# Kernel tuning notes

Hardware: AMD Instinct MI355X
Metric: run time of the kernel (lower is better)

The kernel has to match this reference:

```python
import jax, jax.numpy as jnp
import numpy as np
import math

TOP_K = 10  # top-k codes kept by SOHO_Pre_VD for negative sampling
EPS_LN = 1e-5


def layer_norm(x, w, b):
    mu = jnp.mean(x, axis=-1, keepdims=True)
    var = jnp.mean((x - mu) ** 2, axis=-1, keepdims=True)
    return (x - mu) * jax.lax.rsqrt(var + EPS_LN) * w + b


def position_encoding_sine(b, l, d):
    # mask is all-ones [b, l]; identical across batch, compute once and broadcast
    h = w = int(math.sqrt(l))
    ones = jnp.ones((h, w), jnp.float32)
    y_embed = jnp.cumsum(ones, axis=0)
    x_embed = jnp.cumsum(ones, axis=1)
    eps = 1e-6
    two_pi = 2.0 * np.pi
    y_embed = y_embed / (y_embed[-1:, :] + eps) * two_pi
    x_embed = x_embed / (x_embed[:, -1:] + eps) * two_pi
    pf = d // 2
    dim_t = jnp.arange(pf, dtype=jnp.float32)
    dim_t = 10000.0 ** (2.0 * jnp.floor(dim_t / 2.0) / pf)
    px = x_embed[:, :, None] / dim_t  # [h, w, pf]
    py = y_embed[:, :, None] / dim_t
    # interleave sin(even), cos(odd)
    px = jnp.stack([jnp.sin(px[..., 0::2]), jnp.cos(px[..., 1::2])], axis=-1).reshape(h, w, pf)
    py = jnp.stack([jnp.sin(py[..., 0::2]), jnp.cos(py[..., 1::2])], axis=-1).reshape(h, w, pf)
    pos = jnp.concatenate([py, px], axis=-1).reshape(l, d)  # [l, d]
    return jnp.broadcast_to(pos, (b, l, d))


def setup_inputs() -> dict:
    key = jax.random.key(0)
    ks = jax.random.split(key, 10)
    B, L, CIN, D, K = 16, 576, 1024, 768, 8192
    s = 0.02
    return {
        "img": jax.random.normal(ks[0], (B, L, CIN), jnp.float32),
        "mask_indices": jax.random.randint(ks[1], (B, 1), 0, L),
        "lin_w": jax.random.normal(ks[2], (D, CIN), jnp.float32) * s,
        "lin_b": jnp.zeros((D,), jnp.float32),
        "ln1_w": jnp.ones((D,), jnp.float32),
        "ln1_b": jnp.zeros((D,), jnp.float32),
        "embed": jax.random.normal(ks[3], (K, D), jnp.float32),
        "pos_w": jax.random.normal(ks[4], (D, D), jnp.float32) * s,
        "pos_b": jnp.zeros((D,), jnp.float32),
        "gate_w": jax.random.normal(ks[5], (2, 2 * D), jnp.float32) * s,
        "gate_b": jnp.zeros((2,), jnp.float32),
        "gate_ln_w": jnp.ones((2,), jnp.float32),
        "gate_ln_b": jnp.zeros((2,), jnp.float32),
        "out_ln_w": jnp.ones((D,), jnp.float32),
        "out_ln_b": jnp.zeros((D,), jnp.float32),
    }


def reference(img, mask_indices, lin_w, lin_b, ln1_w, ln1_b, embed, pos_w, pos_b,
              gate_w, gate_b, gate_ln_w, gate_ln_b, out_ln_w, out_ln_b):
    b, l, _ = img.shape
    d = lin_w.shape[0]
    # self.linear: Linear -> LayerNorm -> ReLU
    xq = jax.nn.relu(layer_norm(img @ lin_w.T + lin_b, ln1_w, ln1_b))  # [b,l,d]
    x = xq.reshape(b * l, d)
    # SOHO VQ: nearest code by L2, straight-through
    d2 = (x * x).sum(-1, keepdims=True) - 2.0 * (x @ embed.T) + (embed * embed).sum(-1)  # [N,K]
    idx = jnp.argmin(d2, axis=-1)  # [N]
    quant = jnp.take(embed, idx, axis=0)
    quantized = x + jax.lax.stop_gradient(quant - x)
    probs = jax.nn.softmax(-d2, axis=-1)
    topk_values, topk_indices = jax.lax.top_k(probs, TOP_K)  # [N,K'],[N,K']
    # pos_align linear
    quantized = quantized @ pos_w.T + pos_b
    emb_pt = quantized.reshape(b, l, d)
    # gated fusion
    g = jnp.concatenate([emb_pt, xq], axis=-1) @ gate_w.T + gate_b  # [b,l,2]
    g = jax.nn.relu(layer_norm(g, gate_ln_w, gate_ln_b))
    score = jax.nn.softmax(g, axis=-1)
    emb_s, img_s = score[..., 0:1], score[..., 1:2]
    emb_pt = emb_pt * emb_s + xq * img_s
    pos = position_encoding_sine(b, l, d)
    # negative index construction (visual_mask is all ones)
    ind = idx.reshape(b, l).astype(jnp.float32)  # [b,l]
    masked_labels = jnp.take_along_axis(ind, mask_indices, axis=1)  # [b,1]
    masked_neg = (ind == masked_labels).astype(jnp.float32)[..., None]  # [b,l,1]
    samp = jax.random.categorical(jax.random.key(42), jnp.log(topk_values))  # [N]
    neg = jnp.take_along_axis(topk_indices, samp[:, None], axis=1).reshape(b, l, 1).astype(jnp.float32)
    neg_at_mask = jnp.take_along_axis(neg[..., 0], mask_indices, axis=1)[..., None]  # [b,1,1]
    neg_idx = neg_at_mask * masked_neg + ind[..., None] * (1.0 - masked_neg)  # [b,l,1]
    neg_idx = neg_idx.reshape(b * l).astype(jnp.int32)
    # one-hot matmul == embedding gather
    neg_q = jnp.take(embed, neg_idx, axis=0).reshape(b, l, d)
    neg_q = neg_q * emb_s + jax.lax.stop_gradient(xq) * img_s
    out_pos = layer_norm(emb_pt + pos, out_ln_w, out_ln_b)
    out_neg = layer_norm(neg_q + pos, out_ln_w, out_ln_b)
    return (out_pos, out_neg)
```

## Files before the change

### kernel.cpp

```cpp
#include <hip/hip_runtime.h>
#include <stdint.h>

#define M_TOT  9216
#define D_     768
#define CIN_   1024
#define KCODE  8192
#define TOPK   10

typedef unsigned short u16;
typedef __bf16 bf16x8 __attribute__((ext_vector_type(8)));
typedef float f32x4 __attribute__((ext_vector_type(4)));


__device__ inline float block_sum(float v, float* red) {
    int t = threadIdx.x;
    red[t] = v;
    __syncthreads();
    #pragma unroll
    for (int s = 128; s > 0; s >>= 1) {
        if (t < s) red[t] += red[t + s];
        __syncthreads();
    }
    float r = red[0];
    __syncthreads();
    return r;
}

__device__ inline unsigned long long umin64(unsigned long long a, unsigned long long b) {
    return (a < b) ? a : b;
}

__device__ inline u16 f2bf(float f) {
    uint32_t u = __float_as_uint(f);
    uint32_t r = (u + 0x7fffu + ((u >> 16) & 1u)) >> 16;
    return (u16)r;
}
__device__ inline float bf2f(u16 h) {
    return __uint_as_float(((uint32_t)h) << 16);
}

__device__ inline unsigned long long shfl_xor_u64(unsigned long long v, int mask) {
    int lo = (int)(uint32_t)v, hi = (int)(uint32_t)(v >> 32);
    lo = __shfl_xor(lo, mask, 64);
    hi = __shfl_xor(hi, mask, 64);
    return ((unsigned long long)(uint32_t)hi << 32) | (uint32_t)lo;
}

#define GLDS(gp, lp) __builtin_amdgcn_global_load_lds( \
    (const __attribute__((address_space(1))) unsigned int*)(gp), \
    (__attribute__((address_space(3))) unsigned int*)(lp), 16, 0, 0)


__global__ __launch_bounds__(256) void k_gemm1_mfma(
    const u16* __restrict__ Ah, const u16* __restrict__ Am, const u16* __restrict__ Al,
    const u16* __restrict__ Bh, const u16* __restrict__ Bm, const u16* __restrict__ Bl,
    const float* __restrict__ bias, float* __restrict__ C)
{
    __shared__ __align__(16) u16 sm[24576];
    const int t = threadIdx.x;
    const int lane = t & 63, wid = t >> 6;
    const int row0 = blockIdx.y * 128, col0 = blockIdx.x * 128;
    const int r16 = lane & 15, kb = lane >> 4;
    const int wr = wid >> 1, wc = wid & 1;
    const int sc = (((lane & 3) ^ ((lane >> 3) & 3))) * 8;
    const int lrow = lane >> 2;
    const int swz = (r16 >> 1) & 3;

    f32x4 acc[4][4];
    #pragma unroll
    for (int mf = 0; mf < 4; ++mf)
        #pragma unroll
        for (int nf = 0; nf < 4; ++nf)
            acc[mf][nf] = (f32x4){0.f, 0.f, 0.f, 0.f};

    for (int k0 = 0; k0 < CIN_; k0 += 32) {
        __syncthreads();
        #pragma unroll
        for (int i = 0; i < 12; ++i) {
            int mat = i >> 1;
            int c = (i & 1) ? wid + 4 : wid;
            const u16* mp = (mat == 0) ? Ah : (mat == 1) ? Am : (mat == 2) ? Al
                          : (mat == 3) ? Bh : (mat == 4) ? Bm : Bl;
            int rbase = (mat < 3) ? row0 : col0;
            const u16* g = mp + (size_t)(rbase + c * 16 + lrow) * CIN_ + k0 + sc;
            GLDS(g, sm + mat * 4096 + c * 512);
        }
        __syncthreads();

        const int slot = (kb ^ swz) * 8;
        bf16x8 bh[4], bm[4], bl[4];
        #pragma unroll
        for (int nf = 0; nf < 4; ++nf) {
            int offb = 12288 + (wc * 64 + nf * 16 + r16) * 32 + slot;
            bh[nf] = *(const bf16x8*)(sm + offb);
            bm[nf] = *(const bf16x8*)(sm + offb + 4096);
            bl[nf] = *(const bf16x8*)(sm + offb + 8192);
        }
        #pragma unroll
        for (int mf = 0; mf < 4; ++mf) {
            int offa = (wr * 64 + mf * 16 + r16) * 32 + slot;
            bf16x8 ah = *(const bf16x8*)(sm + offa);
            bf16x8 am = *(const bf16x8*)(sm + offa + 4096);
            bf16x8 al = *(const bf16x8*)(sm + offa + 8192);
            #pragma unroll
            for (int nf = 0; nf < 4; ++nf) {
                acc[mf][nf] = __builtin_amdgcn_mfma_f32_16x16x32_bf16(ah, bh[nf], acc[mf][nf], 0, 0, 0);
                acc[mf][nf] = __builtin_amdgcn_mfma_f32_16x16x32_bf16(ah, bm[nf], acc[mf][nf], 0, 0, 0);
                acc[mf][nf] = __builtin_amdgcn_mfma_f32_16x16x32_bf16(am, bh[nf], acc[mf][nf], 0, 0, 0);
                acc[mf][nf] = __builtin_amdgcn_mfma_f32_16x16x32_bf16(am, bm[nf], acc[mf][nf], 0, 0, 0);
                acc[mf][nf] = __builtin_amdgcn_mfma_f32_16x16x32_bf16(ah, bl[nf], acc[mf][nf], 0, 0, 0);
                acc[mf][nf] = __builtin_amdgcn_mfma_f32_16x16x32_bf16(al, bh[nf], acc[mf][nf], 0, 0, 0);
            }
        }
    }

    #pragma unroll
    for (int mf = 0; mf < 4; ++mf) {
        #pragma unroll
        for (int q = 0; q < 4; ++q) {
            int m = row0 + wr * 64 + mf * 16 + kb * 4 + q;
            #pragma unroll
            for (int nf = 0; nf < 4; ++nf) {
                int n = col0 + wc * 64 + nf * 16 + r16;
                C[(size_t)m * D_ + n] = acc[mf][nf][q] + bias[n];
            }
        }
    }
}

__global__ __launch_bounds__(256) void k_gemm3_mfma(
    const u16* __restrict__ Eh, const u16* __restrict__ El,
    const u16* __restrict__ Ph, const u16* __restrict__ Pl,
    const int* __restrict__ gather,
    const float* __restrict__ bias, float* __restrict__ C)
{
    __shared__ __align__(16) u16 sm[2][16384];
    const int t = threadIdx.x;
    const int lane = t & 63, wid = t >> 6;
    const int row0 = blockIdx.y * 128, col0 = blockIdx.x * 128;
    const int r16 = lane & 15, kb = lane >> 4;
    const int wr = wid >> 1, wc = wid & 1;
    const int sc = (((lane & 3) ^ ((lane >> 3) & 3))) * 8;
    const int lrow = lane >> 2;
    const int swz = (r16 >> 1) & 3;

    const u16* sb = (wid == 0) ? Eh : (wid == 1) ? El : (wid == 2) ? Ph : Pl;
    int grow[8];
    #pragma unroll
    for (int c = 0; c < 8; ++c) {
        int r = ((wid < 2) ? row0 : col0) + c * 16 + lrow;
        grow[c] = (wid < 2) ? gather[r] : r;
    }

    f32x4 acc[4][4];
    #pragma unroll
    for (int mf = 0; mf < 4; ++mf)
        #pragma unroll
        for (int nf = 0; nf < 4; ++nf)
            acc[mf][nf] = (f32x4){0.f, 0.f, 0.f, 0.f};

    auto STAGE = [&](int buf, int k0) {
        u16* dst = sm[buf] + wid * 4096 + lane * 8;
        #pragma unroll
        for (int c = 0; c < 8; ++c)
            GLDS(sb + (size_t)grow[c] * D_ + k0 + sc, dst + c * 512);
    };

    STAGE(0, 0);
    __syncthreads();
    for (int kt = 0; kt < 24; ++kt) {
        int cur = kt & 1;
        if (kt < 23) STAGE(cur ^ 1, (kt + 1) * 32);
        const u16* B = sm[cur];
        const int slot = (kb ^ swz) * 8;
        bf16x8 bh[4], bl[4];
        #pragma unroll
        for (int nf = 0; nf < 4; ++nf) {
            int off = 8192 + (wc * 64 + nf * 16 + r16) * 32 + slot;
            bh[nf] = *(const bf16x8*)(B + off);
            bl[nf] = *(const bf16x8*)(B + off + 4096);
        }
        #pragma unroll
        for (int mf = 0; mf < 4; ++mf) {
            int off = (wr * 64 + mf * 16 + r16) * 32 + slot;
            bf16x8 ah = *(const bf16x8*)(B + off);
            bf16x8 al = *(const bf16x8*)(B + off + 4096);
            #pragma unroll
            for (int nf = 0; nf < 4; ++nf) {
                acc[mf][nf] = __builtin_amdgcn_mfma_f32_16x16x32_bf16(ah, bh[nf], acc[mf][nf], 0, 0, 0);
                acc[mf][nf] = __builtin_amdgcn_mfma_f32_16x16x32_bf16(ah, bl[nf], acc[mf][nf], 0, 0, 0);
                acc[mf][nf] = __builtin_amdgcn_mfma_f32_16x16x32_bf16(al, bh[nf], acc[mf][nf], 0, 0, 0);
            }
        }
        __syncthreads();
    }

    #pragma unroll
    for (int mf = 0; mf < 4; ++mf) {
        #pragma unroll
        for (int q = 0; q < 4; ++q) {
            int m = row0 + wr * 64 + mf * 16 + kb * 4 + q;
            #pragma unroll
            for (int nf = 0; nf < 4; ++nf) {
                int n = col0 + wc * 64 + nf * 16 + r16;
                C[(size_t)m * D_ + n] = acc[mf][nf][q] + bias[n];
            }
        }
    }
}

__global__ void k_rowflag(const int* __restrict__ mask, int* __restrict__ rowflag)
{
    int i = blockIdx.x * 256 + threadIdx.x;
    if (i < M_TOT) {
        int b = i / 576, l = i - b * 576;
        rowflag[i] = (mask[b] == l) ? (b + 1) : 0;
    }
}

__global__ __launch_bounds__(256) void k_gemm2_mfma(
    const u16* __restrict__ Xh, const u16* __restrict__ Xl,
    const u16* __restrict__ Eh, const u16* __restrict__ El,
    const float* __restrict__ xsq, const float* __restrict__ esq,
    const int* __restrict__ rowflag, float* __restrict__ d2row,
    unsigned long long* __restrict__ amin)
{
    __shared__ __align__(16) u16 sm[2][16384];
    const int t = threadIdx.x;
    const int lane = t & 63, wid = t >> 6;
    const int row0 = blockIdx.y * 128, col0 = blockIdx.x * 128;
    const int r16 = lane & 15, kb = lane >> 4;
    const int wr = wid >> 1, wc = wid & 1;
    const int sc = (((lane & 3) ^ ((lane >> 3) & 3))) * 8;
    const int lrow = lane >> 2;
    const int swz = (r16 >> 1) & 3;

    f32x4 acc[4][4];
    #pragma unroll
    for (int mf = 0; mf < 4; ++mf)
        #pragma unroll
        for (int nf = 0; nf < 4; ++nf)
            acc[mf][nf] = (f32x4){0.f, 0.f, 0.f, 0.f};

    const u16* sb = (wid == 0) ? Xh : (wid == 1) ? Xl : (wid == 2) ? Eh : El;
    const int rbase = (wid < 2) ? row0 : col0;
    const u16* srcb = sb + (size_t)(rbase + lrow) * D_ + sc;

    auto STAGE = [&](int buf, int k0) {
        u16* dst = sm[buf] + wid * 4096 + lane * 8;
        #pragma unroll
        for (int c = 0; c < 8; ++c)
            GLDS(srcb + (size_t)c * 16 * D_ + k0, dst + c * 512);
    };

    STAGE(0, 0);
    __syncthreads();
    for (int kt = 0; kt < 24; ++kt) {
        int cur = kt & 1;
        if (kt < 23) STAGE(cur ^ 1, (kt + 1) * 32);
        const u16* B = sm[cur];
        const int slot = (kb ^ swz) * 8;
        bf16x8 bh[4], bl[4];
        #pragma unroll
        for (int nf = 0; nf < 4; ++nf) {
            int off = 8192 + (wc * 64 + nf * 16 + r16) * 32 + slot;
            bh[nf] = *(const bf16x8*)(B + off);
            bl[nf] = *(const bf16x8*)(B + off + 4096);
        }
        #pragma unroll
        for (int mf = 0; mf < 4; ++mf) {
            int off = (wr * 64 + mf * 16 + r16) * 32 + slot;
            bf16x8 ah = *(const bf16x8*)(B + off);
            bf16x8 al = *(const bf16x8*)(B + off + 4096);
            #pragma unroll
            for (int nf = 0; nf < 4; ++nf) {
                acc[mf][nf] = __builtin_amdgcn_mfma_f32_16x16x32_bf16(ah, bh[nf], acc[mf][nf], 0, 0, 0);
                acc[mf][nf] = __builtin_amdgcn_mfma_f32_16x16x32_bf16(ah, bl[nf], acc[mf][nf], 0, 0, 0);
                acc[mf][nf] = __builtin_amdgcn_mfma_f32_16x16x32_bf16(al, bh[nf], acc[mf][nf], 0, 0, 0);
            }
        }
        __syncthreads();
    }

    float esqv[4];
    #pragma unroll
    for (int nf = 0; nf < 4; ++nf)
        esqv[nf] = esq[col0 + wc * 64 + nf * 16 + r16];

    #pragma unroll
    for (int mf = 0; mf < 4; ++mf) {
        #pragma unroll
        for (int q = 0; q < 4; ++q) {
            int m = row0 + wr * 64 + mf * 16 + kb * 4 + q;
            float xsv = xsq[m];
            int rf = rowflag[m];
            unsigned long long best = ~0ull;
            #pragma unroll
            for (int nf = 0; nf < 4; ++nf) {
                int n = col0 + wc * 64 + nf * 16 + r16;
                float d2 = (xsv - 2.0f * acc[mf][nf][q]) + esqv[nf];
                if (rf) d2row[(size_t)(rf - 1) * KCODE + n] = d2;
                unsigned long long key =
                    ((unsigned long long)__float_as_uint(d2) << 32) | (unsigned)n;
                best = umin64(best, key);
            }
            #pragma unroll
            for (int msk = 1; msk < 16; msk <<= 1)
                best = umin64(best, shfl_xor_u64(best, msk));
            if (r16 == 0) atomicMin(&amin[m], best);
        }
    }
}

__global__ __launch_bounds__(256) void k_split3(const float* __restrict__ in,
    u16* __restrict__ h, u16* __restrict__ m, u16* __restrict__ l, int n4)
{
    int i = blockIdx.x * 256 + threadIdx.x;
    int stride = gridDim.x * 256;
    for (; i < n4; i += stride) {
        float4 v = ((const float4*)in)[i];
        ushort4 hv, mv, lv;
        float x, r;
        x = v.x; hv.x = f2bf(x); r = x - bf2f(hv.x); mv.x = f2bf(r); lv.x = f2bf(r - bf2f(mv.x));
        x = v.y; hv.y = f2bf(x); r = x - bf2f(hv.y); mv.y = f2bf(r); lv.y = f2bf(r - bf2f(mv.y));
        x = v.z; hv.z = f2bf(x); r = x - bf2f(hv.z); mv.z = f2bf(r); lv.z = f2bf(r - bf2f(mv.z));
        x = v.w; hv.w = f2bf(x); r = x - bf2f(hv.w); mv.w = f2bf(r); lv.w = f2bf(r - bf2f(mv.w));
        ((ushort4*)h)[i] = hv; ((ushort4*)m)[i] = mv; ((ushort4*)l)[i] = lv;
    }
}

__global__ __launch_bounds__(256) void k_split2(const float* __restrict__ in,
    u16* __restrict__ h, u16* __restrict__ l, int n4)
{
    int i = blockIdx.x * 256 + threadIdx.x;
    int stride = gridDim.x * 256;
    for (; i < n4; i += stride) {
        float4 v = ((const float4*)in)[i];
        ushort4 hv, lv;
        hv.x = f2bf(v.x); lv.x = f2bf(v.x - bf2f(hv.x));
        hv.y = f2bf(v.y); lv.y = f2bf(v.y - bf2f(hv.y));
        hv.z = f2bf(v.z); lv.z = f2bf(v.z - bf2f(hv.z));
        hv.w = f2bf(v.w); lv.w = f2bf(v.w - bf2f(hv.w));
        ((ushort4*)h)[i] = hv; ((ushort4*)l)[i] = lv;
    }
}

__global__ __launch_bounds__(256) void k_ln_relu(
    const float* __restrict__ in, const float* __restrict__ w,
    const float* __restrict__ b, float* __restrict__ xq, float* __restrict__ xsq,
    u16* __restrict__ Xh, u16* __restrict__ Xl)
{
    __shared__ float red[256];
    int r = blockIdx.x, t = threadIdx.x;
    const float* row = in + (size_t)r * D_;
    float v0 = row[t], v1 = row[t + 256], v2 = row[t + 512];
    float mu = block_sum(v0 + v1 + v2, red) * (1.0f / 768.0f);
    float d0 = v0 - mu, d1 = v1 - mu, d2 = v2 - mu;
    float var = block_sum(d0 * d0 + d1 * d1 + d2 * d2, red) * (1.0f / 768.0f);
    float rn = 1.0f / sqrtf(var + 1e-5f);
    float o0 = fmaxf(0.0f, d0 * rn * w[t] + b[t]);
    float o1 = fmaxf(0.0f, d1 * rn * w[t + 256] + b[t + 256]);
    float o2 = fmaxf(0.0f, d2 * rn * w[t + 512] + b[t + 512]);
    float* orow = xq + (size_t)r * D_;
    orow[t] = o0; orow[t + 256] = o1; orow[t + 512] = o2;
    u16 h0 = f2bf(o0), h1 = f2bf(o1), h2 = f2bf(o2);
    Xh[(size_t)r * D_ + t]       = h0;
    Xh[(size_t)r * D_ + t + 256] = h1;
    Xh[(size_t)r * D_ + t + 512] = h2;
    Xl[(size_t)r * D_ + t]       = f2bf(o0 - bf2f(h0));
    Xl[(size_t)r * D_ + t + 256] = f2bf(o1 - bf2f(h1));
    Xl[(size_t)r * D_ + t + 512] = f2bf(o2 - bf2f(h2));
    float q = block_sum(o0 * o0 + o1 * o1 + o2 * o2, red);
    if (t == 0) xsq[r] = q;
}

__global__ __launch_bounds__(256) void k_esq(const float* __restrict__ E,
                                             float* __restrict__ esq,
                                             u16* __restrict__ Eh,
                                             u16* __restrict__ El)
{
    __shared__ float red[256];
    int r = blockIdx.x, t = threadIdx.x;
    const float* row = E + (size_t)r * D_;
    float v0 = row[t], v1 = row[t + 256], v2 = row[t + 512];
    u16 h0 = f2bf(v0), h1 = f2bf(v1), h2 = f2bf(v2);
    Eh[(size_t)r * D_ + t]       = h0;
    Eh[(size_t)r * D_ + t + 256] = h1;
    Eh[(size_t)r * D_ + t + 512] = h2;
    El[(size_t)r * D_ + t]       = f2bf(v0 - bf2f(h0));
    El[(size_t)r * D_ + t + 256] = f2bf(v1 - bf2f(h1));
    El[(size_t)r * D_ + t + 512] = f2bf(v2 - bf2f(h2));
    float s = block_sum(v0 * v0 + v1 * v1 + v2 * v2, red);
    if (t == 0) esq[r] = s;
}

__global__ void k_extract(const unsigned long long* __restrict__ amin,
                          int* __restrict__ idx, int n)
{
    int i = blockIdx.x * 256 + threadIdx.x;
    if (i < n) idx[i] = (int)(amin[i] & 0xFFFFFFFFull);
}

__global__ __launch_bounds__(256) void k_gate(
    const float* __restrict__ embpt, const float* __restrict__ xq,
    const float* __restrict__ gw, const float* __restrict__ gb,
    const float* __restrict__ glnw, const float* __restrict__ glnb,
    float* __restrict__ scores)
{
    __shared__ float red[256];
    int r = blockIdx.x, t = threadIdx.x;
    const float* ep = embpt + (size_t)r * D_;
    const float* xr = xq + (size_t)r * D_;
    float g0 = 0.0f, g1 = 0.0f;
    for (int k = t; k < 1536; k += 256) {
        float v = (k < 768) ? ep[k] : xr[k - 768];
        g0 = fmaf(v, gw[k], g0);
        g1 = fmaf(v, gw[1536 + k], g1);
    }
    g0 = block_sum(g0, red);
    g1 = block_sum(g1, red);
    if (t == 0) {
        g0 += gb[0]; g1 += gb[1];
        float mu = 0.5f * (g0 + g1);
        float h0 = g0 - mu, h1 = g1 - mu;
        float var = 0.5f * (h0 * h0 + h1 * h1);
        float rn = 1.0f / sqrtf(var + 1e-5f);
        float o0 = fmaxf(0.0f, h0 * rn * glnw[0] + glnb[0]);
        float o1 = fmaxf(0.0f, h1 * rn * glnw[1] + glnb[1]);
        float m = fmaxf(o0, o1);
        float e0 = expf(o0 - m), e1 = expf(o1 - m);
        float inv = 1.0f / (e0 + e1);
        scores[r * 2 + 0] = e0 * inv;
        scores[r * 2 + 1] = e1 * inv;
    }
}

__global__ __launch_bounds__(256) void k_pos(float* __restrict__ pos)
{
    int l = blockIdx.x, t = threadIdx.x;
    for (int k = t; k < D_; k += 256) {
        int kk = (k < 384) ? k : k - 384;
        int m = kk >> 1;
        float coord = (k < 384) ? (float)(l / 24) : (float)(l % 24);
        float v = (coord + 1.0f) / 24.000001f * 6.28318530717958647692f;
        float tm = exp2f((float)m * (13.287712379549449f / 192.0f));
        float a = v / tm;
        pos[(size_t)l * D_ + k] = (kk & 1) ? cosf(a) : sinf(a);
    }
}

__device__ inline void threefry2x32(uint32_t x0, uint32_t x1,
                                    uint32_t& o0, uint32_t& o1)
{
    const uint32_t ks0 = 0u, ks1 = 42u;
    const uint32_t ks2 = ks0 ^ ks1 ^ 0x1BD11BDAu;
    uint32_t ks[3] = {ks0, ks1, ks2};
    x0 += ks[0]; x1 += ks[1];
    const int R0[4] = {13, 15, 26, 6};
    const int R1[4] = {17, 29, 16, 24};
    #pragma unroll
    for (int i = 0; i < 5; ++i) {
        const int* R = (i & 1) ? R1 : R0;
        #pragma unroll
        for (int q = 0; q < 4; ++q) {
            x0 += x1;
            x1 = (x1 << R[q]) | (x1 >> (32 - R[q]));
            x1 ^= x0;
        }
        x0 += ks[(i + 1) % 3];
        x1 += ks[(i + 2) % 3] + (uint32_t)(i + 1);
    }
    o0 = x0; o1 = x1;
}

__global__ __launch_bounds__(256) void k_topk_sample(
    const float* __restrict__ d2row, const unsigned long long* __restrict__ amin,
    const int* __restrict__ mask, int* __restrict__ mlabel, int* __restrict__ negsel)
{
    __shared__ float sd2[KCODE];
    __shared__ unsigned long long rbuf[256];
    __shared__ float rfs[256];
    __shared__ int sel[TOPK];
    __shared__ float selv[TOPK];
    __shared__ float sS;
    int b = blockIdx.x, t = threadIdx.x;
    for (int j = t; j < KCODE; j += 256) sd2[j] = d2row[b * KCODE + j];
    __syncthreads();
    for (int p = 0; p < TOPK; ++p) {
        unsigned long long best = ~0ull;
        for (int j = t; j < KCODE; j += 256) {
            bool skip = false;
            for (int q = 0; q < p; ++q) skip = skip || (j == sel[q]);
            if (skip) continue;
            unsigned long long key =
                ((unsigned long long)__float_as_uint(sd2[j]) << 32) | (unsigned)j;
            best = umin64(best, key);
        }
        rbuf[t] = best;
        __syncthreads();
        for (int s = 128; s > 0; s >>= 1) {
            if (t < s) rbuf[t] = umin64(rbuf[t], rbuf[t + s]);
            __syncthreads();
        }
        if (t == 0) {
            sel[p] = (int)(rbuf[0] & 0xFFFFFFFFull);
            selv[p] = __uint_as_float((uint32_t)(rbuf[0] >> 32));
        }
        __syncthreads();
    }
    float d2min = selv[0];
    float part = 0.0f;
    for (int j = t; j < KCODE; j += 256) part += expf(d2min - sd2[j]);
    part = block_sum(part, rfs);
    if (t == 0) sS = part;
    __syncthreads();
    if (t == 0) {
        int rb = b * 576 + mask[b];
        mlabel[b] = (int)(amin[rb] & 0xFFFFFFFFull);
        float S = sS;
        float bestv = 0.0f;
        int samp = 0;
        bool first = true;
        for (int k = 0; k < TOPK; ++k) {
            float pk = expf(d2min - selv[k]) / S;
            float logit = logf(pk);
            unsigned f = (unsigned)(rb * 10 + k);
            uint32_t o0, o1;
            threefry2x32(0u, f, o0, o1);
            uint32_t bits = o0 ^ o1;
            float uu = __uint_as_float(0x3F800000u | (bits >> 9)) - 1.0f;
            uu = uu + 1.1754944e-38f;
            uu = fmaxf(1.1754944e-38f, uu);
            float gum = -logf(-logf(uu));
            float sc = logit + gum;
            if (first || sc > bestv) { bestv = sc; samp = k; first = false; }
        }
        negsel[b] = sel[samp];
    }
}

__global__ __launch_bounds__(256) void k_final(
    const float* __restrict__ embpt, const float* __restrict__ xq,
    const float* __restrict__ scores, const int* __restrict__ idx,
    const int* __restrict__ mlabel, const int* __restrict__ negsel,
    const float* __restrict__ E, const float* __restrict__ pos,
    const float* __restrict__ ow, const float* __restrict__ ob,
    float* __restrict__ outp, float* __restrict__ outn)
{
    __shared__ float red[256];
    int r = blockIdx.x, t = threadIdx.x;
    int b = r / 576, l = r % 576;
    float s0 = scores[r * 2 + 0], s1 = scores[r * 2 + 1];
    int ir = idx[r];
    int nidx = (ir == mlabel[b]) ? negsel[b] : ir;
    const float* ep = embpt + (size_t)r * D_;
    const float* xr = xq + (size_t)r * D_;
    const float* er = E + (size_t)nidx * D_;
    const float* pr = pos + (size_t)l * D_;
    float vp[3], vn[3];
    #pragma unroll
    for (int q = 0; q < 3; ++q) {
        int k = t + q * 256;
        float xv = xr[k] * s1;
        float pv = pr[k];
        vp[q] = (ep[k] * s0 + xv) + pv;
        vn[q] = (er[k] * s0 + xv) + pv;
    }
    float mup = block_sum(vp[0] + vp[1] + vp[2], red) * (1.0f / 768.0f);
    float a0 = vp[0] - mup, a1 = vp[1] - mup, a2 = vp[2] - mup;
    float varp = block_sum(a0 * a0 + a1 * a1 + a2 * a2, red) * (1.0f / 768.0f);
    float rnp = 1.0f / sqrtf(varp + 1e-5f);
    float mun = block_sum(vn[0] + vn[1] + vn[2], red) * (1.0f / 768.0f);
    float c0 = vn[0] - mun, c1 = vn[1] - mun, c2 = vn[2] - mun;
    float varn = block_sum(c0 * c0 + c1 * c1 + c2 * c2, red) * (1.0f / 768.0f);
    float rnn = 1.0f / sqrtf(varn + 1e-5f);
    float* op = outp + (size_t)r * D_;
    float* on = outn + (size_t)r * D_;
    op[t]       = a0 * rnp * ow[t]       + ob[t];
    op[t + 256] = a1 * rnp * ow[t + 256] + ob[t + 256];
    op[t + 512] = a2 * rnp * ow[t + 512] + ob[t + 512];
    on[t]       = c0 * rnn * ow[t]       + ob[t];
    on[t + 256] = c1 * rnn * ow[t + 256] + ob[t + 256];
    on[t + 512] = c2 * rnn * ow[t + 512] + ob[t + 512];
}

extern "C" void kernel_launch(void* const* d_in, const int* in_sizes, int n_in,
                              void* d_out, int out_size, void* d_ws, size_t ws_size,
                              hipStream_t stream)
{
    (void)in_sizes; (void)n_in; (void)out_size; (void)ws_size;
    const float* img    = (const float*)d_in[0];
    const int*   maski  = (const int*)d_in[1];
    const float* lin_w  = (const float*)d_in[2];
    const float* lin_b  = (const float*)d_in[3];
    const float* ln1_w  = (const float*)d_in[4];
    const float* ln1_b  = (const float*)d_in[5];
    const float* embed  = (const float*)d_in[6];
    const float* pos_w  = (const float*)d_in[7];
    const float* pos_b  = (const float*)d_in[8];
    const float* gate_w = (const float*)d_in[9];
    const float* gate_b = (const float*)d_in[10];
    const float* glnw   = (const float*)d_in[11];
    const float* glnb   = (const float*)d_in[12];
    const float* olnw   = (const float*)d_in[13];
    const float* olnb   = (const float*)d_in[14];

    uint8_t* wp = (uint8_t*)d_ws;
    auto alloc = [&](size_t bytes) -> void* {
        void* p = (void*)wp;
        wp += (bytes + 255) & ~(size_t)255;
        return p;
    };
    float* bufA = (float*)alloc((size_t)M_TOT * D_ * 4);
    float* xq   = (float*)alloc((size_t)M_TOT * D_ * 4);
    float* xsq  = (float*)alloc((size_t)M_TOT * 4);
    float* esq  = (float*)alloc((size_t)KCODE * 4);
    unsigned long long* amin = (unsigned long long*)alloc((size_t)M_TOT * 8);
    int*   idxA   = (int*)alloc((size_t)M_TOT * 4);
    int*   rowflag = (int*)alloc((size_t)M_TOT * 4);
    float* scores = (float*)alloc((size_t)M_TOT * 2 * 4);
    float* posb   = (float*)alloc((size_t)576 * D_ * 4);
    float* d2row  = (float*)alloc((size_t)16 * KCODE * 4);
    int*   mlab   = (int*)alloc(16 * 4);
    int*   negsel = (int*)alloc(16 * 4);
    u16* Wh = (u16*)alloc((size_t)D_ * CIN_ * 2);
    u16* Wm = (u16*)alloc((size_t)D_ * CIN_ * 2);
    u16* Wl = (u16*)alloc((size_t)D_ * CIN_ * 2);
    u16* Ph = (u16*)alloc((size_t)D_ * D_ * 2);
    u16* Pl = (u16*)alloc((size_t)D_ * D_ * 2);
    u16* R  = (u16*)alloc((size_t)3 * M_TOT * CIN_ * 2);
    u16* Ih = R;
    u16* Im = R + (size_t)M_TOT * CIN_;
    u16* Il = R + (size_t)2 * M_TOT * CIN_;
    u16* Xh = R;
    u16* Xl = Xh + (size_t)M_TOT * D_;
    u16* Eh = Xl + (size_t)M_TOT * D_;
    u16* El = Eh + (size_t)KCODE * D_;

    float* outp = (float*)d_out;
    float* outn = outp + (size_t)M_TOT * D_;

    hipMemsetAsync(amin, 0xFF, M_TOT * sizeof(unsigned long long), stream);

    dim3 blk(256);
    k_split3<<<2048, blk, 0, stream>>>(img, Ih, Im, Il, M_TOT * CIN_ / 4);
    k_split3<<<768, blk, 0, stream>>>(lin_w, Wh, Wm, Wl, D_ * CIN_ / 4);
    k_split2<<<576, blk, 0, stream>>>(pos_w, Ph, Pl, D_ * D_ / 4);
    k_rowflag<<<M_TOT / 256, blk, 0, stream>>>(maski, rowflag);
    k_gemm1_mfma<<<dim3(D_ / 128, M_TOT / 128), blk, 0, stream>>>(
        Ih, Im, Il, Wh, Wm, Wl, lin_b, bufA);
    k_ln_relu<<<M_TOT, blk, 0, stream>>>(bufA, ln1_w, ln1_b, xq, xsq, Xh, Xl);
    k_esq<<<KCODE, blk, 0, stream>>>(embed, esq, Eh, El);
    k_gemm2_mfma<<<dim3(KCODE / 128, M_TOT / 128), blk, 0, stream>>>(
        Xh, Xl, Eh, El, xsq, esq, rowflag, d2row, amin);
    k_extract<<<M_TOT / 256, blk, 0, stream>>>(amin, idxA, M_TOT);
    k_gemm3_mfma<<<dim3(D_ / 128, M_TOT / 128), blk, 0, stream>>>(
        Eh, El, Ph, Pl, idxA, pos_b, bufA);
    k_gate<<<M_TOT, blk, 0, stream>>>(bufA, xq, gate_w, gate_b, glnw, glnb, scores);
    k_pos<<<576, blk, 0, stream>>>(posb);
    k_topk_sample<<<16, blk, 0, stream>>>(d2row, amin, maski, mlab, negsel);
    k_final<<<M_TOT, blk, 0, stream>>>(bufA, xq, scores, idxA, mlab, negsel,
                                       embed, posb, olnw, olnb, outp, outn);
}
```

Measured before the change: 791.1 us.

## Widen gemm2 K-tile to 64 single-buffered and fuse small prep kernels

The distance GEMM now stages 64-wide K slices into one 64KB LDS buffer, using an 8-way XOR swizzle and two sync points per iteration. This replaces the 32-wide double-buffered pipeline and halves the number of loop iterations and barriers, but loads no longer overlap with compute. Separately, the weight splits and the rowflag kernel are merged into one k_prep launch to cut launch overhead.

```diff
diff --git a/kernel.cpp b/kernel.cpp
--- a/kernel.cpp
+++ b/kernel.cpp
@@ -49,7 +49,6 @@
 #define GLDS(gp, lp) __builtin_amdgcn_global_load_lds( \
     (const __attribute__((address_space(1))) unsigned int*)(gp), \
     (__attribute__((address_space(3))) unsigned int*)(lp), 16, 0, 0)
-
 
 __global__ __launch_bounds__(256) void k_gemm1_mfma(
     const u16* __restrict__ Ah, const u16* __restrict__ Am, const u16* __restrict__ Al,
@@ -209,15 +208,6 @@
     }
 }
 
-__global__ void k_rowflag(const int* __restrict__ mask, int* __restrict__ rowflag)
-{
-    int i = blockIdx.x * 256 + threadIdx.x;
-    if (i < M_TOT) {
-        int b = i / 576, l = i - b * 576;
-        rowflag[i] = (mask[b] == l) ? (b + 1) : 0;
-    }
-}
-
 __global__ __launch_bounds__(256) void k_gemm2_mfma(
     const u16* __restrict__ Xh, const u16* __restrict__ Xl,
     const u16* __restrict__ Eh, const u16* __restrict__ El,
@@ -225,15 +215,12 @@
     const int* __restrict__ rowflag, float* __restrict__ d2row,
     unsigned long long* __restrict__ amin)
 {
-    __shared__ __align__(16) u16 sm[2][16384];
+    __shared__ __align__(16) u16 sm[32768];
     const int t = threadIdx.x;
     const int lane = t & 63, wid = t >> 6;
     const int row0 = blockIdx.y * 128, col0 = blockIdx.x * 128;
     const int r16 = lane & 15, kb = lane >> 4;
     const int wr = wid >> 1, wc = wid & 1;
-    const int sc = (((lane & 3) ^ ((lane >> 3) & 3))) * 8;
-    const int lrow = lane >> 2;
-    const int swz = (r16 >> 1) & 3;
 
     f32x4 acc[4][4];
     #pragma unroll
@@ -244,42 +231,41 @@
 
     const u16* sb = (wid == 0) ? Xh : (wid == 1) ? Xl : (wid == 2) ? Eh : El;
     const int rbase = (wid < 2) ? row0 : col0;
-    const u16* srcb = sb + (size_t)(rbase + lrow) * D_ + sc;
-
-    auto STAGE = [&](int buf, int k0) {
-        u16* dst = sm[buf] + wid * 4096 + lane * 8;
-        #pragma unroll
-        for (int c = 0; c < 8; ++c)
-            GLDS(srcb + (size_t)c * 16 * D_ + k0, dst + c * 512);
-    };
-
-    STAGE(0, 0);
-    __syncthreads();
-    for (int kt = 0; kt < 24; ++kt) {
-        int cur = kt & 1;
-        if (kt < 23) STAGE(cur ^ 1, (kt + 1) * 32);
-        const u16* B = sm[cur];
-        const int slot = (kb ^ swz) * 8;
-        bf16x8 bh[4], bl[4];
-        #pragma unroll
-        for (int nf = 0; nf < 4; ++nf) {
-            int off = 8192 + (wc * 64 + nf * 16 + r16) * 32 + slot;
-            bh[nf] = *(const bf16x8*)(B + off);
-            bl[nf] = *(const bf16x8*)(B + off + 4096);
-        }
-        #pragma unroll
-        for (int mf = 0; mf < 4; ++mf) {
-            int off = (wr * 64 + mf * 16 + r16) * 32 + slot;
-            bf16x8 ah = *(const bf16x8*)(B + off);
-            bf16x8 al = *(const bf16x8*)(B + off + 4096);
+    const u16* srcb = sb + (size_t)(rbase + (lane >> 3)) * D_
+                         + ((lane & 7) ^ (lane >> 3)) * 8;
+    u16* dstb = sm + wid * 8192 + lane * 8;
+
+    const int swz = (r16 & 7);
+    for (int kt = 0; kt < 12; ++kt) {
+        __syncthreads();
+        #pragma unroll
+        for (int c = 0; c < 16; ++c) {
+            GLDS(srcb + kt * 64 + c * 8 * D_, dstb + c * 512);
+        }
+        __syncthreads();
+        #pragma unroll
+        for (int h = 0; h < 2; ++h) {
+            const int slot = ((h * 4 + kb) ^ swz) * 8;
+            bf16x8 bh[4], bl[4];
             #pragma unroll
             for (int nf = 0; nf < 4; ++nf) {
-                acc[mf][nf] = __builtin_amdgcn_mfma_f32_16x16x32_bf16(ah, bh[nf], acc[mf][nf], 0, 0, 0);
-                acc[mf][nf] = __builtin_amdgcn_mfma_f32_16x16x32_bf16(ah, bl[nf], acc[mf][nf], 0, 0, 0);
-                acc[mf][nf] = __builtin_amdgcn_mfma_f32_16x16x32_bf16(al, bh[nf], acc[mf][nf], 0, 0, 0);
+                int off = (wc * 64 + nf * 16 + r16) * 64 + slot;
+                bh[nf] = *(const bf16x8*)(sm + 16384 + off);
+                bl[nf] = *(const bf16x8*)(sm + 24576 + off);
             }
-        }
-        __syncthreads();
+            #pragma unroll
+            for (int mf = 0; mf < 4; ++mf) {
+                int off = (wr * 64 + mf * 16 + r16) * 64 + slot;
+                bf16x8 ah = *(const bf16x8*)(sm + off);
+                bf16x8 al = *(const bf16x8*)(sm + 8192 + off);
+                #pragma unroll
+                for (int nf = 0; nf < 4; ++nf) {
+                    acc[mf][nf] = __builtin_amdgcn_mfma_f32_16x16x32_bf16(ah, bh[nf], acc[mf][nf], 0, 0, 0);
+                    acc[mf][nf] = __builtin_amdgcn_mfma_f32_16x16x32_bf16(ah, bl[nf], acc[mf][nf], 0, 0, 0);
+                    acc[mf][nf] = __builtin_amdgcn_mfma_f32_16x16x32_bf16(al, bh[nf], acc[mf][nf], 0, 0, 0);
+                }
+            }
+        }
     }
 
     float esqv[4];
@@ -329,19 +315,36 @@
     }
 }
 
-__global__ __launch_bounds__(256) void k_split2(const float* __restrict__ in,
-    u16* __restrict__ h, u16* __restrict__ l, int n4)
-{
-    int i = blockIdx.x * 256 + threadIdx.x;
-    int stride = gridDim.x * 256;
-    for (; i < n4; i += stride) {
-        float4 v = ((const float4*)in)[i];
+__global__ __launch_bounds__(256) void k_prep(
+    const float* __restrict__ lin_w, u16* __restrict__ Wh, u16* __restrict__ Wm,
+    u16* __restrict__ Wl,
+    const float* __restrict__ pos_w, u16* __restrict__ Ph, u16* __restrict__ Pl,
+    const int* __restrict__ mask, int* __restrict__ rowflag)
+{
+    int bid = blockIdx.x;
+    if (bid < 768) {
+        int i = bid * 256 + threadIdx.x;
+        float4 v = ((const float4*)lin_w)[i];
+        ushort4 hv, mv, lv;
+        float x, r;
+        x = v.x; hv.x = f2bf(x); r = x - bf2f(hv.x); mv.x = f2bf(r); lv.x = f2bf(r - bf2f(mv.x));
+        x = v.y; hv.y = f2bf(x); r = x - bf2f(hv.y); mv.y = f2bf(r); lv.y = f2bf(r - bf2f(mv.y));
+        x = v.z; hv.z = f2bf(x); r = x - bf2f(hv.z); mv.z = f2bf(r); lv.z = f2bf(r - bf2f(mv.z));
+        x = v.w; hv.w = f2bf(x); r = x - bf2f(hv.w); mv.w = f2bf(r); lv.w = f2bf(r - bf2f(mv.w));
+        ((ushort4*)Wh)[i] = hv; ((ushort4*)Wm)[i] = mv; ((ushort4*)Wl)[i] = lv;
+    } else if (bid < 768 + 576) {
+        int i = (bid - 768) * 256 + threadIdx.x;
+        float4 v = ((const float4*)pos_w)[i];
         ushort4 hv, lv;
         hv.x = f2bf(v.x); lv.x = f2bf(v.x - bf2f(hv.x));
         hv.y = f2bf(v.y); lv.y = f2bf(v.y - bf2f(hv.y));
         hv.z = f2bf(v.z); lv.z = f2bf(v.z - bf2f(hv.z));
         hv.w = f2bf(v.w); lv.w = f2bf(v.w - bf2f(hv.w));
-        ((ushort4*)h)[i] = hv; ((ushort4*)l)[i] = lv;
+        ((ushort4*)Ph)[i] = hv; ((ushort4*)Pl)[i] = lv;
+    } else {
+        int i = (bid - 1344) * 256 + threadIdx.x;
+        int b = i / 576, l = i - b * 576;
+        rowflag[i] = (mask[b] == l) ? (b + 1) : 0;
     }
 }
 
@@ -644,9 +647,7 @@
 
     dim3 blk(256);
     k_split3<<<2048, blk, 0, stream>>>(img, Ih, Im, Il, M_TOT * CIN_ / 4);
-    k_split3<<<768, blk, 0, stream>>>(lin_w, Wh, Wm, Wl, D_ * CIN_ / 4);
-    k_split2<<<576, blk, 0, stream>>>(pos_w, Ph, Pl, D_ * D_ / 4);
-    k_rowflag<<<M_TOT / 256, blk, 0, stream>>>(maski, rowflag);
+    k_prep<<<1380, blk, 0, stream>>>(lin_w, Wh, Wm, Wl, pos_w, Ph, Pl, maski, rowflag);
     k_gemm1_mfma<<<dim3(D_ / 128, M_TOT / 128), blk, 0, stream>>>(
         Ih, Im, Il, Wh, Wm, Wl, lin_b, bufA);
     k_ln_relu<<<M_TOT, blk, 0, stream>>>(bufA, ln1_w, ln1_b, xq, xsq, Xh, Xl);
```

Result: faster. 757.8 us (-4.2%).
